# Kernel optimization log

Hardware: AMD Instinct MI355X
Metric: run time of the kernel (lower is better)

The kernel has to match this reference:

```python
import jax, jax.numpy as jnp
import numpy as np

N_NODES = 10000
N_EDGES = 320000
F = 256


def setup_inputs() -> dict:
    key = jax.random.key(0)
    ks = jax.random.split(key, 8)
    node_feats = jax.random.normal(ks[0], (N_NODES, F), dtype=jnp.float32)
    edge_feats = jax.random.normal(ks[1], (N_EDGES, F), dtype=jnp.float32)
    src = jax.random.randint(ks[2], (N_EDGES,), 0, N_NODES, dtype=jnp.int64)
    dst = jax.random.randint(ks[3], (N_EDGES,), 0, N_NODES, dtype=jnp.int64)
    scale = 1.0 / np.sqrt(F)
    W_src = jax.random.uniform(ks[4], (1, F), jnp.float32, -scale, scale)
    W_dst = jax.random.uniform(ks[5], (1, F), jnp.float32, -scale, scale)
    W_edge = jax.random.uniform(ks[6], (1, F), jnp.float32, -scale, scale)
    b_src = jnp.zeros((1,), jnp.float32)
    b_dst = jnp.zeros((1,), jnp.float32)
    b_edge = jnp.zeros((1,), jnp.float32)
    return {
        "node_feats": node_feats, "edge_feats": edge_feats,
        "src": src, "dst": dst,
        "W_src": W_src, "b_src": b_src,
        "W_dst": W_dst, "b_dst": b_dst,
        "W_edge": W_edge, "b_edge": b_edge,
    }


def reference(node_feats, edge_feats, src, dst,
              W_src, b_src, W_dst, b_dst, W_edge, b_edge):
    # per-node gate projections: [N, out]
    e_src = node_feats @ W_src.T + b_src
    e_dst = node_feats @ W_dst.T + b_dst
    # u_add_v edge gather + edge gate linear, fused elementwise: [E, out]
    m = e_src[src] + e_dst[dst] + (edge_feats @ W_edge.T + b_edge)
    return jax.nn.sigmoid(m)
```

## Files before the change

### kernel.cpp

```cpp
#include <hip/hip_runtime.h>
#include <math.h>


#define FDIM 256
#define F4   (FDIM / 4)

__device__ __forceinline__ float dot4(float4 a, float4 b) {
    return a.x * b.x + a.y * b.y + a.z * b.z + a.w * b.w;
}

__global__ void node_gates_kernel(const float* __restrict__ nf,
                                  const float* __restrict__ W_src,
                                  const float* __restrict__ W_dst,
                                  const float* __restrict__ b_src,
                                  const float* __restrict__ b_dst,
                                  float* __restrict__ e_src,
                                  float* __restrict__ e_dst,
                                  int n_nodes) {
    const int lane   = threadIdx.x & 63;
    const int sub    = lane >> 4;
    const int i      = lane & 15;
    const int wave   = (blockIdx.x * blockDim.x + threadIdx.x) >> 6;
    const int nwaves = (gridDim.x * blockDim.x) >> 6;

    const float4* Ws4 = reinterpret_cast<const float4*>(W_src);
    const float4* Wd4 = reinterpret_cast<const float4*>(W_dst);
    const float4 ws0 = Ws4[i], ws1 = Ws4[i + 16], ws2 = Ws4[i + 32], ws3 = Ws4[i + 48];
    const float4 wd0 = Wd4[i], wd1 = Wd4[i + 16], wd2 = Wd4[i + 32], wd3 = Wd4[i + 48];
    const float bs = b_src[0];
    const float bd = b_dst[0];

    const int ngroups = (n_nodes + 3) >> 2;
    for (int g = wave; g < ngroups; g += nwaves) {
        const int n = g * 4 + sub;
        if (n >= n_nodes) continue;
        const float4* row = reinterpret_cast<const float4*>(nf) + (size_t)n * F4;
        const float4 x0 = row[i], x1 = row[i + 16], x2 = row[i + 32], x3 = row[i + 48];
        float ss = dot4(x0, ws0) + dot4(x1, ws1) + dot4(x2, ws2) + dot4(x3, ws3);
        float sd = dot4(x0, wd0) + dot4(x1, wd1) + dot4(x2, wd2) + dot4(x3, wd3);
        #pragma unroll
        for (int off = 1; off < 16; off <<= 1) {
            ss += __shfl_xor(ss, off, 64);
            sd += __shfl_xor(sd, off, 64);
        }
        if (i == 0) {
            e_src[n] = ss + bs;
            e_dst[n] = sd + bd;
        }
    }
}

__global__ void edge_gate_kernel(const float* __restrict__ ef,
                                 const int* __restrict__ src,
                                 const int* __restrict__ dst,
                                 const float* __restrict__ W_edge,
                                 const float* __restrict__ b_edge,
                                 const float* __restrict__ e_src,
                                 const float* __restrict__ e_dst,
                                 float* __restrict__ out,
                                 int n_edges) {
    const int lane   = threadIdx.x & 63;
    const int sub    = lane >> 4;
    const int i      = lane & 15;
    const int wave   = (blockIdx.x * blockDim.x + threadIdx.x) >> 6;
    const int nwaves = (gridDim.x * blockDim.x) >> 6;

    const float4* We4 = reinterpret_cast<const float4*>(W_edge);
    const float4 w0 = We4[i], w1 = We4[i + 16], w2 = We4[i + 32], w3 = We4[i + 48];
    const float be = b_edge[0];

    const int ngroups = (n_edges + 3) >> 2;
    for (int g = wave; g < ngroups; g += nwaves) {
        const int e = g * 4 + sub;
        if (e >= n_edges) continue;
        const float4* row = reinterpret_cast<const float4*>(ef) + (size_t)e * F4;
        const float4 x0 = row[i], x1 = row[i + 16], x2 = row[i + 32], x3 = row[i + 48];
        float s = dot4(x0, w0) + dot4(x1, w1) + dot4(x2, w2) + dot4(x3, w3);
        #pragma unroll
        for (int off = 1; off < 16; off <<= 1) {
            s += __shfl_xor(s, off, 64);
        }
        if (i == 0) {
            const float m = s + be + e_src[src[e]] + e_dst[dst[e]];
            out[e] = 1.0f / (1.0f + expf(-m));
        }
    }
}

extern "C" void kernel_launch(void* const* d_in, const int* in_sizes, int n_in,
                              void* d_out, int out_size, void* d_ws, size_t ws_size,
                              hipStream_t stream) {
    const float* node_feats = (const float*)d_in[0];
    const float* edge_feats = (const float*)d_in[1];
    const int*   src        = (const int*)d_in[2];
    const int*   dst        = (const int*)d_in[3];
    const float* W_src      = (const float*)d_in[4];
    const float* b_src      = (const float*)d_in[5];
    const float* W_dst      = (const float*)d_in[6];
    const float* b_dst      = (const float*)d_in[7];
    const float* W_edge     = (const float*)d_in[8];
    const float* b_edge     = (const float*)d_in[9];

    const int n_nodes = in_sizes[0] / FDIM;
    const int n_edges = in_sizes[2];

    float* e_src = (float*)d_ws;
    float* e_dst = e_src + n_nodes;

    {
        int ngroups = (n_nodes + 3) / 4;
        int blocks = (ngroups + 3) / 4;
        if (blocks > 2048) blocks = 2048;
        node_gates_kernel<<<blocks, 256, 0, stream>>>(
            node_feats, W_src, W_dst, b_src, b_dst, e_src, e_dst, n_nodes);
    }

    {
        int blocks = 2048;
        edge_gate_kernel<<<blocks, 256, 0, stream>>>(
            edge_feats, src, dst, W_edge, b_edge, e_src, e_dst,
            (float*)d_out, n_edges);
    }
}
```

Before: 62.78 us.

## Fuse node and edge phases into one cooperative kernel with grid sync

Measured after the change: 155.9 us. 2.48x slower.

```diff
diff --git a/kernel.cpp b/kernel.cpp
--- a/kernel.cpp
+++ b/kernel.cpp
@@ -1,5 +1,8 @@
 #include <hip/hip_runtime.h>
+#include <hip/hip_cooperative_groups.h>
 #include <math.h>
+
+namespace cg = cooperative_groups;
 
 
 #define FDIM 256
@@ -9,20 +12,15 @@
     return a.x * b.x + a.y * b.y + a.z * b.z + a.w * b.w;
 }
 
-__global__ void node_gates_kernel(const float* __restrict__ nf,
-                                  const float* __restrict__ W_src,
-                                  const float* __restrict__ W_dst,
-                                  const float* __restrict__ b_src,
-                                  const float* __restrict__ b_dst,
-                                  float* __restrict__ e_src,
-                                  float* __restrict__ e_dst,
-                                  int n_nodes) {
-    const int lane   = threadIdx.x & 63;
-    const int sub    = lane >> 4;
-    const int i      = lane & 15;
-    const int wave   = (blockIdx.x * blockDim.x + threadIdx.x) >> 6;
-    const int nwaves = (gridDim.x * blockDim.x) >> 6;
-
+__device__ __forceinline__ void node_phase(const float* __restrict__ nf,
+                                           const float* __restrict__ W_src,
+                                           const float* __restrict__ W_dst,
+                                           const float* __restrict__ b_src,
+                                           const float* __restrict__ b_dst,
+                                           float* __restrict__ e_src,
+                                           float* __restrict__ e_dst,
+                                           int n_nodes, int wave, int nwaves,
+                                           int sub, int i) {
     const float4* Ws4 = reinterpret_cast<const float4*>(W_src);
     const float4* Wd4 = reinterpret_cast<const float4*>(W_dst);
     const float4 ws0 = Ws4[i], ws1 = Ws4[i + 16], ws2 = Ws4[i + 32], ws3 = Ws4[i + 48];
@@ -50,21 +48,16 @@
     }
 }
 
-__global__ void edge_gate_kernel(const float* __restrict__ ef,
-                                 const int* __restrict__ src,
-                                 const int* __restrict__ dst,
-                                 const float* __restrict__ W_edge,
-                                 const float* __restrict__ b_edge,
-                                 const float* __restrict__ e_src,
-                                 const float* __restrict__ e_dst,
-                                 float* __restrict__ out,
-                                 int n_edges) {
-    const int lane   = threadIdx.x & 63;
-    const int sub    = lane >> 4;
-    const int i      = lane & 15;
-    const int wave   = (blockIdx.x * blockDim.x + threadIdx.x) >> 6;
-    const int nwaves = (gridDim.x * blockDim.x) >> 6;
-
+__device__ __forceinline__ void edge_phase(const float* __restrict__ ef,
+                                           const int* __restrict__ src,
+                                           const int* __restrict__ dst,
+                                           const float* __restrict__ W_edge,
+                                           const float* __restrict__ b_edge,
+                                           const float* __restrict__ e_src,
+                                           const float* __restrict__ e_dst,
+                                           float* __restrict__ out,
+                                           int n_edges, int wave, int nwaves,
+                                           int sub, int i) {
     const float4* We4 = reinterpret_cast<const float4*>(W_edge);
     const float4 w0 = We4[i], w1 = We4[i + 16], w2 = We4[i + 32], w3 = We4[i + 48];
     const float be = b_edge[0];
@@ -87,6 +80,58 @@
     }
 }
 
+__global__ void __launch_bounds__(256, 8)
+fused_kernel(const float* __restrict__ nf, const float* __restrict__ ef,
+             const int* __restrict__ src, const int* __restrict__ dst,
+             const float* __restrict__ W_src, const float* __restrict__ b_src,
+             const float* __restrict__ W_dst, const float* __restrict__ b_dst,
+             const float* __restrict__ W_edge, const float* __restrict__ b_edge,
+             float* __restrict__ e_src, float* __restrict__ e_dst,
+             float* __restrict__ out, int n_nodes, int n_edges) {
+    const int lane   = threadIdx.x & 63;
+    const int sub    = lane >> 4;
+    const int i      = lane & 15;
+    const int wave   = (blockIdx.x * blockDim.x + threadIdx.x) >> 6;
+    const int nwaves = (gridDim.x * blockDim.x) >> 6;
+
+    node_phase(nf, W_src, W_dst, b_src, b_dst, e_src, e_dst,
+               n_nodes, wave, nwaves, sub, i);
+    cg::this_grid().sync();
+    edge_phase(ef, src, dst, W_edge, b_edge, e_src, e_dst, out,
+               n_edges, wave, nwaves, sub, i);
+}
+
+__global__ void node_gates_kernel(const float* __restrict__ nf,
+                                  const float* __restrict__ W_src,
+                                  const float* __restrict__ W_dst,
+                                  const float* __restrict__ b_src,
+                                  const float* __restrict__ b_dst,
+                                  float* __restrict__ e_src,
+                                  float* __restrict__ e_dst,
+                                  int n_nodes) {
+    const int lane   = threadIdx.x & 63;
+    const int wave   = (blockIdx.x * blockDim.x + threadIdx.x) >> 6;
+    const int nwaves = (gridDim.x * blockDim.x) >> 6;
+    node_phase(nf, W_src, W_dst, b_src, b_dst, e_src, e_dst,
+               n_nodes, wave, nwaves, lane >> 4, lane & 15);
+}
+
+__global__ void edge_gate_kernel(const float* __restrict__ ef,
+                                 const int* __restrict__ src,
+                                 const int* __restrict__ dst,
+                                 const float* __restrict__ W_edge,
+                                 const float* __restrict__ b_edge,
+                                 const float* __restrict__ e_src,
+                                 const float* __restrict__ e_dst,
+                                 float* __restrict__ out,
+                                 int n_edges) {
+    const int lane   = threadIdx.x & 63;
+    const int wave   = (blockIdx.x * blockDim.x + threadIdx.x) >> 6;
+    const int nwaves = (gridDim.x * blockDim.x) >> 6;
+    edge_phase(ef, src, dst, W_edge, b_edge, e_src, e_dst, out,
+               n_edges, wave, nwaves, lane >> 4, lane & 15);
+}
+
 extern "C" void kernel_launch(void* const* d_in, const int* in_sizes, int n_in,
                               void* d_out, int out_size, void* d_ws, size_t ws_size,
                               hipStream_t stream) {
@@ -106,6 +151,28 @@
 
     float* e_src = (float*)d_ws;
     float* e_dst = e_src + n_nodes;
+    float* outp  = (float*)d_out;
+
+    int occ = 0;
+    hipError_t err = hipOccupancyMaxActiveBlocksPerMultiprocessor(
+        &occ, fused_kernel, 256, 0);
+    if (err == hipSuccess && occ > 0) {
+        int blocks = occ * 256;
+        if (blocks > 2048) blocks = 2048;
+        void* args[] = {
+            (void*)&node_feats, (void*)&edge_feats,
+            (void*)&src, (void*)&dst,
+            (void*)&W_src, (void*)&b_src,
+            (void*)&W_dst, (void*)&b_dst,
+            (void*)&W_edge, (void*)&b_edge,
+            (void*)&e_src, (void*)&e_dst,
+            (void*)&outp, (void*)&n_nodes, (void*)&n_edges,
+        };
+        err = hipLaunchCooperativeKernel((void*)fused_kernel,
+                                         dim3(blocks), dim3(256),
+                                         args, 0, stream);
+        if (err == hipSuccess) return;
+    }
 
     {
         int ngroups = (n_nodes + 3) / 4;
@@ -114,11 +181,9 @@
         node_gates_kernel<<<blocks, 256, 0, stream>>>(
             node_feats, W_src, W_dst, b_src, b_dst, e_src, e_dst, n_nodes);
     }
-
     {
-        int blocks = 2048;
-        edge_gate_kernel<<<blocks, 256, 0, stream>>>(
+        edge_gate_kernel<<<2048, 256, 0, stream>>>(
             edge_feats, src, dst, W_edge, b_edge, e_src, e_dst,
-            (float*)d_out, n_edges);
+            outp, n_edges);
     }
 }
```

## Software-pipeline edge feature loads with nontemporal prefetch of next row group

Applied to the files above, without the earlier changes.

Measured after the change: 59.48 us. -5.2%, faster.

```diff
diff --git a/kernel.cpp b/kernel.cpp
--- a/kernel.cpp
+++ b/kernel.cpp
@@ -3,10 +3,12 @@
 
 
 #define FDIM 256
-#define F4   (FDIM / 4)
+#define F4   64
 
-__device__ __forceinline__ float dot4(float4 a, float4 b) {
-    return a.x * b.x + a.y * b.y + a.z * b.z + a.w * b.w;
+typedef float f32x4 __attribute__((ext_vector_type(4)));
+
+__device__ __forceinline__ float dot4v(f32x4 a, f32x4 b) {
+    return a[0] * b[0] + a[1] * b[1] + a[2] * b[2] + a[3] * b[3];
 }
 
 __global__ void node_gates_kernel(const float* __restrict__ nf,
@@ -23,10 +25,10 @@
     const int wave   = (blockIdx.x * blockDim.x + threadIdx.x) >> 6;
     const int nwaves = (gridDim.x * blockDim.x) >> 6;
 
-    const float4* Ws4 = reinterpret_cast<const float4*>(W_src);
-    const float4* Wd4 = reinterpret_cast<const float4*>(W_dst);
-    const float4 ws0 = Ws4[i], ws1 = Ws4[i + 16], ws2 = Ws4[i + 32], ws3 = Ws4[i + 48];
-    const float4 wd0 = Wd4[i], wd1 = Wd4[i + 16], wd2 = Wd4[i + 32], wd3 = Wd4[i + 48];
+    const f32x4* Ws4 = reinterpret_cast<const f32x4*>(W_src);
+    const f32x4* Wd4 = reinterpret_cast<const f32x4*>(W_dst);
+    const f32x4 ws0 = Ws4[i], ws1 = Ws4[i + 16], ws2 = Ws4[i + 32], ws3 = Ws4[i + 48];
+    const f32x4 wd0 = Wd4[i], wd1 = Wd4[i + 16], wd2 = Wd4[i + 32], wd3 = Wd4[i + 48];
     const float bs = b_src[0];
     const float bd = b_dst[0];
 
@@ -34,10 +36,10 @@
     for (int g = wave; g < ngroups; g += nwaves) {
         const int n = g * 4 + sub;
         if (n >= n_nodes) continue;
-        const float4* row = reinterpret_cast<const float4*>(nf) + (size_t)n * F4;
-        const float4 x0 = row[i], x1 = row[i + 16], x2 = row[i + 32], x3 = row[i + 48];
-        float ss = dot4(x0, ws0) + dot4(x1, ws1) + dot4(x2, ws2) + dot4(x3, ws3);
-        float sd = dot4(x0, wd0) + dot4(x1, wd1) + dot4(x2, wd2) + dot4(x3, wd3);
+        const f32x4* row = reinterpret_cast<const f32x4*>(nf) + (size_t)n * F4;
+        const f32x4 x0 = row[i], x1 = row[i + 16], x2 = row[i + 32], x3 = row[i + 48];
+        float ss = dot4v(x0, ws0) + dot4v(x1, ws1) + dot4v(x2, ws2) + dot4v(x3, ws3);
+        float sd = dot4v(x0, wd0) + dot4v(x1, wd1) + dot4v(x2, wd2) + dot4v(x3, wd3);
         #pragma unroll
         for (int off = 1; off < 16; off <<= 1) {
             ss += __shfl_xor(ss, off, 64);
@@ -50,40 +52,75 @@
     }
 }
 
-__global__ void edge_gate_kernel(const float* __restrict__ ef,
-                                 const int* __restrict__ src,
-                                 const int* __restrict__ dst,
-                                 const float* __restrict__ W_edge,
-                                 const float* __restrict__ b_edge,
-                                 const float* __restrict__ e_src,
-                                 const float* __restrict__ e_dst,
-                                 float* __restrict__ out,
-                                 int n_edges) {
+__global__ void __launch_bounds__(256, 8)
+edge_gate_kernel(const float* __restrict__ ef,
+                 const int* __restrict__ src,
+                 const int* __restrict__ dst,
+                 const float* __restrict__ W_edge,
+                 const float* __restrict__ b_edge,
+                 const float* __restrict__ e_src,
+                 const float* __restrict__ e_dst,
+                 float* __restrict__ out,
+                 int n_edges) {
     const int lane   = threadIdx.x & 63;
     const int sub    = lane >> 4;
     const int i      = lane & 15;
     const int wave   = (blockIdx.x * blockDim.x + threadIdx.x) >> 6;
     const int nwaves = (gridDim.x * blockDim.x) >> 6;
 
-    const float4* We4 = reinterpret_cast<const float4*>(W_edge);
-    const float4 w0 = We4[i], w1 = We4[i + 16], w2 = We4[i + 32], w3 = We4[i + 48];
+    const f32x4* We4 = reinterpret_cast<const f32x4*>(W_edge);
+    const f32x4 w0 = We4[i], w1 = We4[i + 16], w2 = We4[i + 32], w3 = We4[i + 48];
     const float be = b_edge[0];
 
+    const f32x4* ef4 = reinterpret_cast<const f32x4*>(ef);
     const int ngroups = (n_edges + 3) >> 2;
-    for (int g = wave; g < ngroups; g += nwaves) {
+
+    int g = wave;
+    if (g >= ngroups) return;
+
+    f32x4 x0, x1, x2, x3;
+    {
         const int e = g * 4 + sub;
-        if (e >= n_edges) continue;
-        const float4* row = reinterpret_cast<const float4*>(ef) + (size_t)e * F4;
-        const float4 x0 = row[i], x1 = row[i + 16], x2 = row[i + 32], x3 = row[i + 48];
-        float s = dot4(x0, w0) + dot4(x1, w1) + dot4(x2, w2) + dot4(x3, w3);
+        if (e < n_edges) {
+            const f32x4* row = ef4 + (size_t)e * F4;
+            x0 = __builtin_nontemporal_load(row + i);
+            x1 = __builtin_nontemporal_load(row + i + 16);
+            x2 = __builtin_nontemporal_load(row + i + 32);
+            x3 = __builtin_nontemporal_load(row + i + 48);
+        } else {
+            x0 = x1 = x2 = x3 = (f32x4)0.f;
+        }
+    }
+
+    while (g < ngroups) {
+        const int gn = g + nwaves;
+        f32x4 y0, y1, y2, y3;
+        if (gn < ngroups) {
+            const int en = gn * 4 + sub;
+            if (en < n_edges) {
+                const f32x4* row = ef4 + (size_t)en * F4;
+                y0 = __builtin_nontemporal_load(row + i);
+                y1 = __builtin_nontemporal_load(row + i + 16);
+                y2 = __builtin_nontemporal_load(row + i + 32);
+                y3 = __builtin_nontemporal_load(row + i + 48);
+            } else {
+                y0 = y1 = y2 = y3 = (f32x4)0.f;
+            }
+        }
+
+        float s = dot4v(x0, w0) + dot4v(x1, w1) + dot4v(x2, w2) + dot4v(x3, w3);
         #pragma unroll
         for (int off = 1; off < 16; off <<= 1) {
             s += __shfl_xor(s, off, 64);
         }
-        if (i == 0) {
+        const int e = g * 4 + sub;
+        if (i == 0 && e < n_edges) {
             const float m = s + be + e_src[src[e]] + e_dst[dst[e]];
-            out[e] = 1.0f / (1.0f + expf(-m));
+            out[e] = 1.0f / (1.0f + __expf(-m));
         }
+
+        g = gn;
+        x0 = y0; x1 = y1; x2 = y2; x3 = y3;
     }
 }
 
@@ -116,8 +153,7 @@
     }
 
     {
-        int blocks = 2048;
-        edge_gate_kernel<<<blocks, 256, 0, stream>>>(
+        edge_gate_kernel<<<2048, 256, 0, stream>>>(
             edge_feats, src, dst, W_edge, b_edge, e_src, e_dst,
             (float*)d_out, n_edges);
     }
```
